# Performance work log

Hardware: AMD Instinct MI355X
Metric: run time of the kernel (lower is better)

## Reference

```python
import jax, jax.numpy as jnp
import numpy as np
from jax import lax

B = 128
HW = 80
NUM_RES_BLOCKS = 3
PC_DIM = 8          # primary capsule dim
PC_CH = 16          # primary capsule channels
DC_DIM = 16         # digit capsule dim
NUM_CLASSES = 10
NUM_PRIMARY = PC_CH * 9 * 9  # 1296


def setup_inputs() -> dict:
    key = jax.random.key(0)
    ks = jax.random.split(key, 16)
    d = {}
    d['x'] = jax.random.normal(ks[0], (B, 1, HW, HW), dtype=jnp.float32)
    # conv1: Conv2d(1, 32, k=3, s=1, p=1) with bias
    d['conv1_w'] = jax.random.normal(ks[1], (32, 1, 3, 3), dtype=jnp.float32) * 0.1
    d['conv1_b'] = jnp.zeros((32,), dtype=jnp.float32)
    d['bn1_g'] = jnp.ones((32,), dtype=jnp.float32)
    d['bn1_b'] = jnp.zeros((32,), dtype=jnp.float32)
    # residual blocks (stacked over block dim): conv1 is 1x1, conv2 is 3x3 pad 1, both bias-free
    d['rb_c1_w'] = jax.random.normal(ks[2], (NUM_RES_BLOCKS, 32, 32, 1, 1), dtype=jnp.float32) * 0.05
    d['rb_bn1_g'] = jnp.ones((NUM_RES_BLOCKS, 32), dtype=jnp.float32)
    d['rb_bn1_b'] = jnp.zeros((NUM_RES_BLOCKS, 32), dtype=jnp.float32)
    d['rb_c2_w'] = jax.random.normal(ks[3], (NUM_RES_BLOCKS, 32, 32, 3, 3), dtype=jnp.float32) * 0.05
    d['rb_bn2_g'] = jnp.ones((NUM_RES_BLOCKS, 32), dtype=jnp.float32)
    d['rb_bn2_b'] = jnp.zeros((NUM_RES_BLOCKS, 32), dtype=jnp.float32)
    # primary capsules: Conv2d(32, 16*8=128, k=9, s=8) with bias
    d['pcaps_w'] = jax.random.normal(ks[4], (PC_CH * PC_DIM, 32, 9, 9), dtype=jnp.float32) * 0.02
    d['pcaps_b'] = jnp.zeros((PC_CH * PC_DIM,), dtype=jnp.float32)
    # routing weights W: original shape (1, 1296, 10, 16, 8); drop broadcast batch dim
    d['W_caps'] = 0.01 * jax.random.normal(ks[5], (NUM_PRIMARY, NUM_CLASSES, DC_DIM, PC_DIM), dtype=jnp.float32)
    return d


def _conv(x, w, stride=1, pad=0):
    return lax.conv_general_dilated(
        x, w, (stride, stride), [(pad, pad), (pad, pad)],
        dimension_numbers=('NCHW', 'OIHW', 'NCHW'))


def _bn(x, g, b, eps=1e-5):
    # training-mode batch norm (batch statistics, biased variance)
    m = jnp.mean(x, axis=(0, 2, 3), keepdims=True)
    v = jnp.var(x, axis=(0, 2, 3), keepdims=True)
    return (x - m) * lax.rsqrt(v + eps) * g[None, :, None, None] + b[None, :, None, None]


def _squash(s, axis=-1):
    n2 = jnp.sum(s * s, axis=axis, keepdims=True)
    return (n2 / (1.0 + n2)) * (s / jnp.sqrt(n2 + 1e-9))


def reference(x, conv1_w, conv1_b, bn1_g, bn1_b,
              rb_c1_w, rb_bn1_g, rb_bn1_b, rb_c2_w, rb_bn2_g, rb_bn2_b,
              pcaps_w, pcaps_b, W_caps):
    h = _conv(x, conv1_w, stride=1, pad=1) + conv1_b[None, :, None, None]
    h = jax.nn.relu(_bn(h, bn1_g, bn1_b))
    for i in range(NUM_RES_BLOCKS):
        idt = h
        o = jax.nn.relu(_bn(_conv(h, rb_c1_w[i]), rb_bn1_g[i], rb_bn1_b[i]))
        o = _bn(_conv(o, rb_c2_w[i], pad=1), rb_bn2_g[i], rb_bn2_b[i])
        h = jax.nn.relu(o + idt)
    # primary capsules -> [B, 128, 9, 9]
    p = _conv(h, pcaps_w, stride=8) + pcaps_b[None, :, None, None]
    bsz = p.shape[0]
    p = p.reshape(bsz, PC_CH, PC_DIM, 9, 9)
    p = jnp.transpose(p, (0, 1, 3, 4, 2)).reshape(bsz, NUM_PRIMARY, PC_DIM)  # [B, 1296, 8]
    # u_hat[b,p,c,d] = W[p,c,d,k] * u[b,p,k]
    u_hat = jnp.einsum('pcdk,bpk->bpcd', W_caps, p)  # [B, 1296, 10, 16]
    # dynamic routing, 3 iterations
    b_log = jnp.zeros((bsz, NUM_PRIMARY, NUM_CLASSES), dtype=u_hat.dtype)
    for r in range(3):
        c = jax.nn.softmax(b_log, axis=2)  # [B, 1296, 10]
        s = jnp.einsum('bpc,bpcd->bcd', c, u_hat)  # [B, 10, 16]
        v = _squash(s, axis=-1)
        if r < 2:
            b_log = b_log + jnp.einsum('bpcd,bcd->bpc', u_hat, v)
    lengths = jnp.sqrt(jnp.sum(v * v, axis=-1) + 1e-9)  # [B, 10]
    return (v, lengths)
```

## Files before the change

kernel.cpp:

```cpp
#include <hip/hip_runtime.h>
#include <hip/hip_bf16.h>
#include <cstddef>


#define B_ 128
#define HW_ 80
#define PIX 6400
#define CHW 204800
#define NPRIM 1296

typedef __attribute__((ext_vector_type(8))) short bf16x8;
typedef __attribute__((ext_vector_type(4))) float f32x4;

__device__ inline float ldH(const unsigned short* p, size_t i) {
  union { unsigned int u; float f; } c; c.u = ((unsigned int)p[i]) << 16; return c.f;
}
__device__ inline float bf16tof(unsigned short u) {
  union { unsigned int uu; float f; } c; c.uu = ((unsigned int)u) << 16; return c.f;
}
__device__ inline float lo16f(unsigned int w) {
  union { unsigned int uu; float f; } c; c.uu = w << 16; return c.f;
}
__device__ inline float hi16f(unsigned int w) {
  union { unsigned int uu; float f; } c; c.uu = w & 0xffff0000u; return c.f;
}
__device__ inline unsigned short ftobf16(float v) {
  __hip_bfloat16 b = __float2bfloat16(v);
  return *reinterpret_cast<unsigned short*>(&b);
}
__device__ inline float stRound(float* p, size_t i, float v) { p[i] = v; return v; }
__device__ inline float stRound(unsigned short* p, size_t i, float v) {
  unsigned short u = ftobf16(v); p[i] = u; return bf16tof(u);
}

__global__ __launch_bounds__(256) void conv1_k(const float* __restrict__ x,
                                               const float* __restrict__ w,
                                               const float* __restrict__ bias,
                                               unsigned short* __restrict__ out,
                                               float* __restrict__ partc) {
  __shared__ float sAB[4 * 64];
  int idx = blockIdx.x * 256 + threadIdx.x;
  int b = idx / PIX, p = idx - b * PIX;
  int y = p / HW_, xx = p - y * HW_;
  const float* xb = x + (size_t)b * PIX;
  float in[3][3];
#pragma unroll
  for (int dy = 0; dy < 3; dy++) {
    int yy = y + dy - 1;
#pragma unroll
    for (int dx = 0; dx < 3; dx++) {
      int xc = xx + dx - 1;
      in[dy][dx] = (yy >= 0 && yy < HW_ && xc >= 0 && xc < HW_) ? xb[yy * HW_ + xc] : 0.f;
    }
  }
  int lane = threadIdx.x & 63, wv = threadIdx.x >> 6;
  size_t obase = (size_t)b * CHW + p;
#pragma unroll 1
  for (int co = 0; co < 32; co++) {
    float a = bias[co];
#pragma unroll
    for (int t = 0; t < 9; t++) a = fmaf(in[t / 3][t % 3], w[co * 9 + t], a);
    float ar = stRound(out, obase + (size_t)co * PIX, a);
    float r = ar, r2 = ar * ar;
#pragma unroll
    for (int off = 32; off > 0; off >>= 1) { r += __shfl_down(r, off); r2 += __shfl_down(r2, off); }
    if (lane == 0) { sAB[wv * 64 + co] = r; sAB[wv * 64 + 32 + co] = r2; }
  }
  __syncthreads();
  if (threadIdx.x < 64) {
    float s = sAB[threadIdx.x] + sAB[64 + threadIdx.x] + sAB[128 + threadIdx.x] + sAB[192 + threadIdx.x];
    partc[(size_t)blockIdx.x * 64 + threadIdx.x] = s;
  }
}

__global__ __launch_bounds__(256) void finC_k(const float* __restrict__ partc,
                                              const float* __restrict__ g,
                                              const float* __restrict__ bb,
                                              float* __restrict__ sb) {
  __shared__ float red[256];
  int co = blockIdx.x;
  int tid = threadIdx.x;
  int half = tid >> 7, t = tid & 127;
  const float* p = partc + (half ? (32 + co) : co);
  float s = 0.f;
  for (int j = t; j < 3200; j += 128) s += p[(size_t)j * 64];
  red[tid] = s;
  __syncthreads();
  for (int st = 64; st > 0; st >>= 1) {
    if (t < st) red[half * 128 + t] += red[half * 128 + t + st];
    __syncthreads();
  }
  if (tid == 0) {
    float sum = red[0], sum2 = red[128];
    const float inv = 1.f / 819200.f;
    float mean = sum * inv;
    float var = sum2 * inv - mean * mean;
    float sc = g[co] * rsqrtf(var + 1e-5f);
    sb[co] = sc;
    sb[32 + co] = bb[co] - mean * sc;
  }
}

template <bool RES, bool STATS1>
__global__ __launch_bounds__(256) void fuse_k(const unsigned short* __restrict__ X,
                                              const unsigned short* __restrict__ Hold,
                                              unsigned short* __restrict__ Hout,
                                              unsigned int* __restrict__ Xa4,
                                              const float* __restrict__ sb,
                                              const float* __restrict__ w1,
                                              float* __restrict__ partc) {
  __shared__ float sAB[4 * 64];
  int idx = blockIdx.x * 256 + threadIdx.x;
  int b = idx / PIX, p = idx - b * PIX;
  size_t base = (size_t)b * CHW + p;
  float h[32];
#pragma unroll
  for (int ci = 0; ci < 32; ci++) {
    float v = bf16tof(X[base + (size_t)ci * PIX]);
    v = fmaf(v, sb[ci], sb[32 + ci]);
    if (RES) v += ldH(Hold, base + (size_t)ci * PIX);
    v = fmaxf(v, 0.f);
    h[ci] = stRound(Hout, base + (size_t)ci * PIX, v);
  }
  if (STATS1) {
    int lane = threadIdx.x & 63, wv = threadIdx.x >> 6;
    unsigned int pk[16];
#pragma unroll
    for (int co = 0; co < 32; co++) {
      float a = 0.f;
#pragma unroll
      for (int ci = 0; ci < 32; ci++) a = fmaf(h[ci], w1[co * 32 + ci], a);
      unsigned short ua = ftobf16(a);
      if (co & 1) pk[co >> 1] |= ((unsigned int)ua) << 16;
      else        pk[co >> 1] = (unsigned int)ua;
      float ar = bf16tof(ua);
      float r = ar, r2 = ar * ar;
#pragma unroll
      for (int off = 32; off > 0; off >>= 1) { r += __shfl_down(r, off); r2 += __shfl_down(r2, off); }
      if (lane == 0) { sAB[wv * 64 + co] = r; sAB[wv * 64 + 32 + co] = r2; }
    }
    uint4* dst = (uint4*)(Xa4 + ((size_t)b * PIX + p) * 16);
#pragma unroll
    for (int q = 0; q < 4; q++) {
      uint4 v;
      v.x = pk[q * 4 + 0]; v.y = pk[q * 4 + 1]; v.z = pk[q * 4 + 2]; v.w = pk[q * 4 + 3];
      dst[q] = v;
    }
    __syncthreads();
    if (threadIdx.x < 64) {
      float s = sAB[threadIdx.x] + sAB[64 + threadIdx.x] + sAB[128 + threadIdx.x] + sAB[192 + threadIdx.x];
      partc[(size_t)blockIdx.x * 64 + threadIdx.x] = s;
    }
  }
}

__global__ __launch_bounds__(256) void wprep_k(const float* __restrict__ pw,
                                               const float* __restrict__ rb3,
                                               unsigned short* __restrict__ wpc,
                                               float* __restrict__ wp) {
  int idx = blockIdx.x * 256 + threadIdx.x;
  if (idx < 331776) {
    int j = idx & 7, co = (idx >> 3) & 127, lg = (idx >> 10) & 3, s = idx >> 12;
    int ci = lg * 8 + j;
    float w = pw[(size_t)co * 2592 + ci * 81 + s];
    unsigned short hi = ftobf16(w);
    wpc[idx] = hi;
    wpc[331776 + idx] = ftobf16(w - bf16tof(hi));
  } else if (idx < 359424) {
    int e2 = idx - 331776;
    int rb = e2 / 9216, e = e2 - rb * 9216;
    unsigned short* wA3 = (unsigned short*)(wp + rb * 9216);
    int j = e & 7, co = (e >> 3) & 31, g = (e >> 8) & 3, t = e >> 10;
    int ci = g * 8 + j;
    float w = rb3[rb * 9216 + (co * 32 + ci) * 9 + t];
    unsigned short hi = ftobf16(w);
    wA3[e] = hi;
    wA3[9216 + e] = ftobf16(w - bf16tof(hi));
  }
}

__global__ __launch_bounds__(256) void conv3_k(const unsigned int* __restrict__ Xa4,
                                               const float* __restrict__ sba,
                                               const unsigned short* __restrict__ wA3,
                                               unsigned short* __restrict__ X,
                                               float* __restrict__ partc) {
  __shared__ unsigned int o1s[16 * 330];
  __shared__ float sAB[4 * 64];
  int tile_id = blockIdx.x;
  int ty0 = (tile_id / 5) * 16, tx0 = (tile_id % 5) * 16;
  int b = blockIdx.y;
  size_t ibase = (size_t)b * CHW;

  for (int px = threadIdx.x; px < 324; px += 256) {
    int iy = px / 18, ix = px - iy * 18;
    int gy = ty0 - 1 + iy, gx = tx0 - 1 + ix;
    bool inimg = (gy >= 0 && gy < HW_ && gx >= 0 && gx < HW_);
    if (inimg) {
      const uint4* src = (const uint4*)(Xa4 + ((size_t)b * PIX + gy * HW_ + gx) * 16);
      uint4 q0 = src[0], q1 = src[1], q2 = src[2], q3 = src[3];
      unsigned int raw[16] = {q0.x, q0.y, q0.z, q0.w, q1.x, q1.y, q1.z, q1.w,
                              q2.x, q2.y, q2.z, q2.w, q3.x, q3.y, q3.z, q3.w};
#pragma unroll
      for (int pr = 0; pr < 16; pr++) {
        float a0 = lo16f(raw[pr]);
        float a1 = hi16f(raw[pr]);
        float o0 = fmaxf(fmaf(a0, sba[2 * pr], sba[32 + 2 * pr]), 0.f);
        float o1v = fmaxf(fmaf(a1, sba[2 * pr + 1], sba[32 + 2 * pr + 1]), 0.f);
        o1s[pr * 330 + px] = (unsigned int)ftobf16(o0) | ((unsigned int)ftobf16(o1v) << 16);
      }
    } else {
#pragma unroll
      for (int pr = 0; pr < 16; pr++) o1s[pr * 330 + px] = 0u;
    }
  }
  __syncthreads();

  int lane = threadIdx.x & 63;
  int wid = threadIdx.x >> 6;
  int l15 = lane & 15, lg = lane >> 4;

  f32x4 acc8[8];
#pragma unroll
  for (int u = 0; u < 8; u++) acc8[u] = f32x4{0.f, 0.f, 0.f, 0.f};

#pragma unroll 1
  for (int t = 0; t < 9; t++) {
    int dy = t / 3, dx = t - dy * 3;
    int abase = ((t * 4 + lg) * 32 + l15) * 8;
    bf16x8 ah0 = *reinterpret_cast<const bf16x8*>(wA3 + abase);
    bf16x8 ah1 = *reinterpret_cast<const bf16x8*>(wA3 + abase + 128);
    bf16x8 al0 = *reinterpret_cast<const bf16x8*>(wA3 + 9216 + abase);
    bf16x8 al1 = *reinterpret_cast<const bf16x8*>(wA3 + 9216 + abase + 128);
#pragma unroll
    for (int s = 0; s < 4; s++) {
      int hpx = (wid * 4 + s + dy) * 18 + l15 + dx;
      int wbase = lg * 4 * 330 + hpx;
      union { unsigned int u[4]; bf16x8 v; } bb;
      bb.u[0] = o1s[wbase];
      bb.u[1] = o1s[wbase + 330];
      bb.u[2] = o1s[wbase + 660];
      bb.u[3] = o1s[wbase + 990];
      acc8[s * 2 + 0] = __builtin_amdgcn_mfma_f32_16x16x32_bf16(ah0, bb.v, acc8[s * 2 + 0], 0, 0, 0);
      acc8[s * 2 + 0] = __builtin_amdgcn_mfma_f32_16x16x32_bf16(al0, bb.v, acc8[s * 2 + 0], 0, 0, 0);
      acc8[s * 2 + 1] = __builtin_amdgcn_mfma_f32_16x16x32_bf16(ah1, bb.v, acc8[s * 2 + 1], 0, 0, 0);
      acc8[s * 2 + 1] = __builtin_amdgcn_mfma_f32_16x16x32_bf16(al1, bb.v, acc8[s * 2 + 1], 0, 0, 0);
    }
  }

  float sacc[2][4], s2acc[2][4];
#pragma unroll
  for (int Mt = 0; Mt < 2; Mt++)
#pragma unroll
    for (int r = 0; r < 4; r++) { sacc[Mt][r] = 0.f; s2acc[Mt][r] = 0.f; }

  int gx = tx0 + l15;
#pragma unroll
  for (int s = 0; s < 4; s++) {
    int gy = ty0 + wid * 4 + s;
#pragma unroll
    for (int Mt = 0; Mt < 2; Mt++) {
#pragma unroll
      for (int r = 0; r < 4; r++) {
        unsigned short uv = ftobf16(acc8[s * 2 + Mt][r]);
        int co = Mt * 16 + lg * 4 + r;
        X[ibase + (size_t)co * PIX + gy * HW_ + gx] = uv;
        float vr = bf16tof(uv);
        sacc[Mt][r] += vr; s2acc[Mt][r] += vr * vr;
      }
    }
  }
#pragma unroll
  for (int off = 1; off < 16; off <<= 1) {
#pragma unroll
    for (int Mt = 0; Mt < 2; Mt++)
#pragma unroll
      for (int r = 0; r < 4; r++) {
        sacc[Mt][r] += __shfl_xor(sacc[Mt][r], off);
        s2acc[Mt][r] += __shfl_xor(s2acc[Mt][r], off);
      }
  }
  if (l15 == 0) {
#pragma unroll
    for (int Mt = 0; Mt < 2; Mt++)
#pragma unroll
      for (int r = 0; r < 4; r++) {
        int co = Mt * 16 + lg * 4 + r;
        sAB[wid * 64 + co] = sacc[Mt][r];
        sAB[wid * 64 + 32 + co] = s2acc[Mt][r];
      }
  }
  __syncthreads();
  if (threadIdx.x < 64) {
    float s = sAB[threadIdx.x] + sAB[64 + threadIdx.x] + sAB[128 + threadIdx.x] + sAB[192 + threadIdx.x];
    partc[((size_t)(b * 25 + tile_id)) * 64 + threadIdx.x] = s;
  }
}

__global__ __launch_bounds__(256) void pcapsm_k(const unsigned short* __restrict__ Hb,
                                                const unsigned short* __restrict__ wpc,
                                                const float* __restrict__ bias,
                                                float* __restrict__ P) {
  __shared__ unsigned int hs[16 * 721];
  int oy = blockIdx.x, b = blockIdx.y;
  for (int i = threadIdx.x; i < 11520; i += 256) {
    int pr = i / 720, rem = i - pr * 720;
    int ky = rem / 80, col = rem - ky * 80;
    size_t src = ((size_t)(b * 32 + 2 * pr) * HW_ + oy * 8 + ky) * HW_ + col;
    unsigned int pk = (unsigned int)Hb[src] | ((unsigned int)Hb[src + PIX] << 16);
    int phys = (col & 7) * 10 + (col >> 3);
    hs[pr * 721 + ky * 80 + phys] = pk;
  }
  __syncthreads();

  int lane = threadIdx.x & 63, wid = threadIdx.x >> 6;
  int l15 = lane & 15, lg = lane >> 4;
  int colb = (l15 < 9) ? l15 * 8 : (l15 - 9) * 8 + 4;

  f32x4 acc[2];
  acc[0] = f32x4{0.f, 0.f, 0.f, 0.f};
  acc[1] = f32x4{0.f, 0.f, 0.f, 0.f};

#pragma unroll 3
  for (int s = 0; s < 81; s++) {
    int ky = s / 9, kx = s - ky * 9;
    int c = colb + kx;
    int phys = (c & 7) * 10 + (c >> 3);
    int wb = ky * 80 + phys;
    union { unsigned int u[4]; bf16x8 v; } bb;
    bb.u[0] = hs[(lg * 4 + 0) * 721 + wb];
    bb.u[1] = hs[(lg * 4 + 1) * 721 + wb];
    bb.u[2] = hs[(lg * 4 + 2) * 721 + wb];
    bb.u[3] = hs[(lg * 4 + 3) * 721 + wb];
#pragma unroll
    for (int m = 0; m < 2; m++) {
      int mt = wid * 2 + m;
      size_t ab = ((size_t)(s * 4 + lg) * 128 + mt * 16 + l15) * 8;
      bf16x8 ahi = *reinterpret_cast<const bf16x8*>(wpc + ab);
      bf16x8 alo = *reinterpret_cast<const bf16x8*>(wpc + 331776 + ab);
      acc[m] = __builtin_amdgcn_mfma_f32_16x16x32_bf16(ahi, bb.v, acc[m], 0, 0, 0);
      acc[m] = __builtin_amdgcn_mfma_f32_16x16x32_bf16(alo, bb.v, acc[m], 0, 0, 0);
    }
  }

  int ox = l15;
  if (ox < 9) {
#pragma unroll
    for (int m = 0; m < 2; m++) {
      int mt = wid * 2 + m;
#pragma unroll
      for (int r = 0; r < 4; r++) {
        int co = mt * 16 + lg * 4 + r;
        int pp = (co >> 3) * 81 + oy * 9 + ox;
        P[((size_t)b * NPRIM + pp) * 8 + (co & 7)] = acc[m][r] + bias[co];
      }
    }
  }
}

__global__ __launch_bounds__(256) void uhat_k(const float* __restrict__ Pp,
                                              const float* __restrict__ W,
                                              unsigned short* __restrict__ UH) {
  int p = blockIdx.x;
  __shared__ __align__(16) float ush[1024];
  for (int i = threadIdx.x; i < 1024; i += 256) {
    int b = i >> 3, k = i & 7;
    ush[i] = Pp[((size_t)b * NPRIM + p) * 8 + k];
  }
  int cdq = threadIdx.x & 31, bg = threadIdx.x >> 5;
  float4 w0[5], w1[5];
#pragma unroll
  for (int j = 0; j < 5; j++) {
    const float4* wp = (const float4*)(W + ((size_t)p * 160 + j * 32 + cdq) * 8);
    w0[j] = wp[0]; w1[j] = wp[1];
  }
  __syncthreads();
#pragma unroll 1
  for (int pass = 0; pass < 16; pass++) {
    int b = pass * 8 + bg;
    const float4* up = (const float4*)(ush + b * 8);
    float4 u0 = up[0], u1 = up[1];
#pragma unroll
    for (int j = 0; j < 5; j++) {
      float a = w0[j].x * u0.x + w0[j].y * u0.y + w0[j].z * u0.z + w0[j].w * u0.w +
                w1[j].x * u1.x + w1[j].y * u1.y + w1[j].z * u1.z + w1[j].w * u1.w;
      UH[((size_t)b * NPRIM + p) * 160 + j * 32 + cdq] = ftobf16(a);
    }
  }
}

__global__ __launch_bounds__(256) void sred0_k(const unsigned short* __restrict__ UH,
                                               float* __restrict__ V) {
  int c = blockIdx.x, b = blockIdx.y;
  int d = threadIdx.x & 15, pg = threadIdx.x >> 4;
  float acc = 0.f;
  for (int p = pg; p < NPRIM; p += 16)
    acc += 0.1f * bf16tof(UH[((size_t)b * NPRIM + p) * 160 + c * 16 + d]);
  __shared__ float red[256];
  red[threadIdx.x] = acc;
  __syncthreads();
  for (int st = 128; st >= 16; st >>= 1) {
    if (threadIdx.x < st) red[threadIdx.x] += red[threadIdx.x + st];
    __syncthreads();
  }
  if (threadIdx.x < 16) {
    float sv = red[threadIdx.x];
    float n2 = sv * sv;
#pragma unroll
    for (int off = 1; off < 16; off <<= 1) n2 += __shfl_xor(n2, off);
    float sc = (n2 / (1.f + n2)) / sqrtf(n2 + 1e-9f);
    V[((size_t)b * 10 + c) * 16 + threadIdx.x] = sv * sc;
  }
}

template <bool FIRST>
__global__ __launch_bounds__(256) void route_k(const unsigned short* __restrict__ UH,
                                               const float* __restrict__ V,
                                               const float* __restrict__ blogin,
                                               float* __restrict__ blogout,
                                               float* __restrict__ SPART) {
  __shared__ float cl[10 * 216];
  __shared__ float vsh[160];
  int seg = blockIdx.x, b = blockIdx.y;
  for (int i = threadIdx.x; i < 160; i += 256) vsh[i] = V[(size_t)b * 160 + i];
  __syncthreads();
  int pl = threadIdx.x;
  if (pl < 216) {
    int p = seg * 216 + pl;
    const uint4* uh4 = (const uint4*)(UH + ((size_t)b * NPRIM + p) * 160);
    float t[10];
#pragma unroll
    for (int c = 0; c < 10; c++) t[c] = 0.f;
#pragma unroll
    for (int j = 0; j < 20; j++) {
      uint4 u = uh4[j];
      int c = j >> 1, d0 = (j & 1) * 8;
      const float* vs = vsh + c * 16 + d0;
      t[c] += lo16f(u.x) * vs[0] + hi16f(u.x) * vs[1] +
              lo16f(u.y) * vs[2] + hi16f(u.y) * vs[3] +
              lo16f(u.z) * vs[4] + hi16f(u.z) * vs[5] +
              lo16f(u.w) * vs[6] + hi16f(u.w) * vs[7];
    }
    if (!FIRST) {
      const float* bi = blogin + ((size_t)b * NPRIM + p) * 10;
#pragma unroll
      for (int c = 0; c < 10; c++) t[c] += bi[c];
    }
    float* bo = blogout + ((size_t)b * NPRIM + p) * 10;
#pragma unroll
    for (int c = 0; c < 10; c++) bo[c] = t[c];
    float mx = -3.4e38f;
#pragma unroll
    for (int c = 0; c < 10; c++) mx = fmaxf(mx, t[c]);
    float sum = 0.f;
    float e[10];
#pragma unroll
    for (int c = 0; c < 10; c++) { e[c] = __expf(t[c] - mx); sum += e[c]; }
    float inv = 1.f / sum;
#pragma unroll
    for (int c = 0; c < 10; c++) cl[c * 216 + pl] = e[c] * inv;
  }
  __syncthreads();
  if (threadIdx.x < 160) {
    int c = threadIdx.x >> 4, d = threadIdx.x & 15;
    const unsigned short* uhc = UH + ((size_t)b * NPRIM + seg * 216) * 160 + c * 16 + d;
    float s = 0.f;
#pragma unroll 4
    for (int q = 0; q < 216; q++) s += cl[c * 216 + q] * bf16tof(uhc[(size_t)q * 160]);
    SPART[((size_t)b * 6 + seg) * 160 + threadIdx.x] = s;
  }
}

template <bool FINAL>
__global__ __launch_bounds__(256) void squashred_k(const float* __restrict__ SPART,
                                                   float* __restrict__ V,
                                                   float* __restrict__ out) {
  int b = blockIdx.x;
  int t = threadIdx.x;
  if (t < 160) {
    float s = 0.f;
#pragma unroll
    for (int seg = 0; seg < 6; seg++) s += SPART[((size_t)b * 6 + seg) * 160 + t];
    float n2 = s * s;
#pragma unroll
    for (int off = 1; off < 16; off <<= 1) n2 += __shfl_xor(n2, off);
    float sc = (n2 / (1.f + n2)) / sqrtf(n2 + 1e-9f);
    float v = s * sc;
    if (FINAL) {
      out[(size_t)b * 160 + t] = v;
      if ((t & 15) == 0) out[20480 + b * 10 + (t >> 4)] = sqrtf(n2 * sc * sc + 1e-9f);
    } else {
      V[(size_t)b * 160 + t] = v;
    }
  }
}

extern "C" void kernel_launch(void* const* d_in, const int* in_sizes, int n_in,
                              void* d_out, int out_size, void* d_ws, size_t ws_size,
                              hipStream_t stream) {
  (void)in_sizes; (void)n_in; (void)out_size; (void)ws_size;
  const float* x        = (const float*)d_in[0];
  const float* conv1_w  = (const float*)d_in[1];
  const float* conv1_b  = (const float*)d_in[2];
  const float* bn1_g    = (const float*)d_in[3];
  const float* bn1_b    = (const float*)d_in[4];
  const float* rb_c1_w  = (const float*)d_in[5];
  const float* rb_bn1_g = (const float*)d_in[6];
  const float* rb_bn1_b = (const float*)d_in[7];
  const float* rb_c2_w  = (const float*)d_in[8];
  const float* rb_bn2_g = (const float*)d_in[9];
  const float* rb_bn2_b = (const float*)d_in[10];
  const float* pcaps_w  = (const float*)d_in[11];
  const float* pcaps_b  = (const float*)d_in[12];
  const float* W_caps   = (const float*)d_in[13];
  float* ws  = (float*)d_ws;
  float* out = (float*)d_out;

  unsigned short* Xb = (unsigned short*)ws;
  unsigned short* Hb = (unsigned short*)(ws + 13107200);
  unsigned int* Xa4  = (unsigned int*)(ws + 26214400);
  unsigned short* WPC = (unsigned short*)(ws + 52428800);
  float* PART = ws + 52428800 + 331776;
  float* SB   = PART + 32768;
  float* P    = SB + 512;
  float* BLOG = P + 1327104;
  float* WP    = P;
  float* PARTC = BLOG;
  unsigned short* UH = (unsigned short*)(ws + 2654208);
  float* SPART = P;
  float* V     = BLOG + 1658880 + 20480;

  wprep_k<<<1404, 256, 0, stream>>>(pcaps_w, rb_c2_w, WPC, WP);
  conv1_k<<<3200, 256, 0, stream>>>(x, conv1_w, conv1_b, Xb, PARTC);
  finC_k<<<32, 256, 0, stream>>>(PARTC, bn1_g, bn1_b, SB + 0);
  fuse_k<false, true><<<3200, 256, 0, stream>>>(Xb, nullptr, Hb, Xa4, SB + 0,
                                                rb_c1_w + 0, PARTC);
  finC_k<<<32, 256, 0, stream>>>(PARTC, rb_bn1_g + 0, rb_bn1_b + 0, SB + 1 * 64);

  for (int i = 0; i < 3; i++) {
    int sa = 1 + 2 * i, sx = 2 + 2 * i;
    conv3_k<<<dim3(25, 128), 256, 0, stream>>>(Xa4, SB + sa * 64,
                                               (unsigned short*)(WP + i * 9216),
                                               Xb, PARTC);
    finC_k<<<32, 256, 0, stream>>>(PARTC, rb_bn2_g + i * 32, rb_bn2_b + i * 32, SB + sx * 64);
    if (i < 2) {
      fuse_k<true, true><<<3200, 256, 0, stream>>>(Xb, Hb, Hb, Xa4, SB + sx * 64,
                                                   rb_c1_w + (i + 1) * 1024, PARTC);
      finC_k<<<32, 256, 0, stream>>>(PARTC, rb_bn1_g + (i + 1) * 32, rb_bn1_b + (i + 1) * 32,
                                     SB + (sx + 1) * 64);
    } else {
      fuse_k<true, false><<<3200, 256, 0, stream>>>(Xb, Hb, Hb, nullptr, SB + sx * 64,
                                                    nullptr, nullptr);
    }
  }

  pcapsm_k<<<dim3(9, 128), 256, 0, stream>>>(Hb, WPC, pcaps_b, P);
  uhat_k<<<1296, 256, 0, stream>>>(P, W_caps, UH);

  sred0_k<<<dim3(10, 128), 256, 0, stream>>>(UH, V);
  route_k<true><<<dim3(6, 128), 256, 0, stream>>>(UH, V, nullptr, BLOG, SPART);
  squashred_k<false><<<128, 256, 0, stream>>>(SPART, V, nullptr);
  route_k<false><<<dim3(6, 128), 256, 0, stream>>>(UH, V, BLOG, BLOG, SPART);
  squashred_k<true><<<128, 256, 0, stream>>>(SPART, nullptr, out);
}
```

Baseline: 711.7 us.

## Compute residual 1x1 conv with bf16 split-precision MFMA in fuse kernel

Replaces the per-thread scalar 32x32 FMA loop for the 1x1 conv in fuse_k with MFMA 16x16x32 bf16 instructions. Activations are staged through shared memory, and weights are pre-split into hi/lo bf16 pairs by wprep_k to keep near-fp32 accuracy. BN statistics are now reduced with xor shuffles over 16 lanes instead of a full-wave reduction per output channel. The intent is to remove the heavy scalar FMA and shuffle work, at the cost of extra LDS traffic, a second barrier, and a changed workspace layout for the weights.

Result: faster. 587.7 us (-17.4%).

```diff
diff --git a/kernel.cpp b/kernel.cpp
--- a/kernel.cpp
+++ b/kernel.cpp
@@ -107,10 +107,10 @@
                                               unsigned short* __restrict__ Hout,
                                               unsigned int* __restrict__ Xa4,
                                               const float* __restrict__ sb,
-                                              const float* __restrict__ w1,
+                                              const unsigned short* __restrict__ wf1,
                                               float* __restrict__ partc) {
-  __shared__ float sAB[4 * 64];
-  int idx = blockIdx.x * 256 + threadIdx.x;
+  int tid = threadIdx.x;
+  int idx = blockIdx.x * 256 + tid;
   int b = idx / PIX, p = idx - b * PIX;
   size_t base = (size_t)b * CHW + p;
   float h[32];
@@ -123,39 +123,106 @@
     h[ci] = stRound(Hout, base + (size_t)ci * PIX, v);
   }
   if (STATS1) {
-    int lane = threadIdx.x & 63, wv = threadIdx.x >> 6;
-    unsigned int pk[16];
-#pragma unroll
-    for (int co = 0; co < 32; co++) {
-      float a = 0.f;
-#pragma unroll
-      for (int ci = 0; ci < 32; ci++) a = fmaf(h[ci], w1[co * 32 + ci], a);
-      unsigned short ua = ftobf16(a);
-      if (co & 1) pk[co >> 1] |= ((unsigned int)ua) << 16;
-      else        pk[co >> 1] = (unsigned int)ua;
-      float ar = bf16tof(ua);
-      float r = ar, r2 = ar * ar;
-#pragma unroll
-      for (int off = 32; off > 0; off >>= 1) { r += __shfl_down(r, off); r2 += __shfl_down(r2, off); }
-      if (lane == 0) { sAB[wv * 64 + co] = r; sAB[wv * 64 + 32 + co] = r2; }
-    }
-    uint4* dst = (uint4*)(Xa4 + ((size_t)b * PIX + p) * 16);
-#pragma unroll
-    for (int q = 0; q < 4; q++) {
-      uint4 v;
-      v.x = pk[q * 4 + 0]; v.y = pk[q * 4 + 1]; v.z = pk[q * 4 + 2]; v.w = pk[q * 4 + 3];
-      dst[q] = v;
+    __shared__ unsigned int hls[16 * 260];
+    __shared__ float sAB[4 * 64];
+#pragma unroll
+    for (int pr = 0; pr < 16; pr++) {
+      unsigned int pk = (unsigned int)ftobf16(h[2 * pr]) |
+                        ((unsigned int)ftobf16(h[2 * pr + 1]) << 16);
+      hls[pr * 260 + tid] = pk;
     }
     __syncthreads();
-    if (threadIdx.x < 64) {
-      float s = sAB[threadIdx.x] + sAB[64 + threadIdx.x] + sAB[128 + threadIdx.x] + sAB[192 + threadIdx.x];
-      partc[(size_t)blockIdx.x * 64 + threadIdx.x] = s;
+
+    int lane = tid & 63, wv = tid >> 6;
+    int l15 = lane & 15, lg = (lane >> 4) & 3;
+    int pbase = p - tid;
+
+    bf16x8 ah[2], al[2];
+#pragma unroll
+    for (int mt = 0; mt < 2; mt++) {
+      size_t ab = ((size_t)(mt * 4 + lg) * 16 + l15) * 8;
+      ah[mt] = *reinterpret_cast<const bf16x8*>(wf1 + ab);
+      al[mt] = *reinterpret_cast<const bf16x8*>(wf1 + 1024 + ab);
+    }
+
+    f32x4 acc[4][2];
+#pragma unroll
+    for (int nt = 0; nt < 4; nt++)
+#pragma unroll
+      for (int mt = 0; mt < 2; mt++) acc[nt][mt] = f32x4{0.f, 0.f, 0.f, 0.f};
+
+#pragma unroll
+    for (int nt = 0; nt < 4; nt++) {
+      int px = wv * 64 + nt * 16 + l15;
+      union { unsigned int u[4]; bf16x8 v; } bb;
+      bb.u[0] = hls[(lg * 4 + 0) * 260 + px];
+      bb.u[1] = hls[(lg * 4 + 1) * 260 + px];
+      bb.u[2] = hls[(lg * 4 + 2) * 260 + px];
+      bb.u[3] = hls[(lg * 4 + 3) * 260 + px];
+#pragma unroll
+      for (int mt = 0; mt < 2; mt++) {
+        acc[nt][mt] = __builtin_amdgcn_mfma_f32_16x16x32_bf16(ah[mt], bb.v, acc[nt][mt], 0, 0, 0);
+        acc[nt][mt] = __builtin_amdgcn_mfma_f32_16x16x32_bf16(al[mt], bb.v, acc[nt][mt], 0, 0, 0);
+      }
+    }
+
+    float sacc[2][4], s2acc[2][4];
+#pragma unroll
+    for (int mt = 0; mt < 2; mt++)
+#pragma unroll
+      for (int r = 0; r < 4; r++) { sacc[mt][r] = 0.f; s2acc[mt][r] = 0.f; }
+
+#pragma unroll
+    for (int nt = 0; nt < 4; nt++) {
+      int px = wv * 64 + nt * 16 + l15;
+      size_t xb4 = ((size_t)b * PIX + pbase + px) * 16;
+#pragma unroll
+      for (int mt = 0; mt < 2; mt++) {
+        unsigned short u0 = ftobf16(acc[nt][mt][0]);
+        unsigned short u1 = ftobf16(acc[nt][mt][1]);
+        unsigned short u2 = ftobf16(acc[nt][mt][2]);
+        unsigned short u3 = ftobf16(acc[nt][mt][3]);
+        int pi = mt * 8 + lg * 2;
+        Xa4[xb4 + pi] = (unsigned int)u0 | ((unsigned int)u1 << 16);
+        Xa4[xb4 + pi + 1] = (unsigned int)u2 | ((unsigned int)u3 << 16);
+        float v0 = bf16tof(u0), v1 = bf16tof(u1), v2 = bf16tof(u2), v3 = bf16tof(u3);
+        sacc[mt][0] += v0; s2acc[mt][0] += v0 * v0;
+        sacc[mt][1] += v1; s2acc[mt][1] += v1 * v1;
+        sacc[mt][2] += v2; s2acc[mt][2] += v2 * v2;
+        sacc[mt][3] += v3; s2acc[mt][3] += v3 * v3;
+      }
+    }
+#pragma unroll
+    for (int off = 1; off < 16; off <<= 1) {
+#pragma unroll
+      for (int mt = 0; mt < 2; mt++)
+#pragma unroll
+        for (int r = 0; r < 4; r++) {
+          sacc[mt][r] += __shfl_xor(sacc[mt][r], off);
+          s2acc[mt][r] += __shfl_xor(s2acc[mt][r], off);
+        }
+    }
+    if (l15 == 0) {
+#pragma unroll
+      for (int mt = 0; mt < 2; mt++)
+#pragma unroll
+        for (int r = 0; r < 4; r++) {
+          int co = mt * 16 + lg * 4 + r;
+          sAB[wv * 64 + co] = sacc[mt][r];
+          sAB[wv * 64 + 32 + co] = s2acc[mt][r];
+        }
+    }
+    __syncthreads();
+    if (tid < 64) {
+      float s = sAB[tid] + sAB[64 + tid] + sAB[128 + tid] + sAB[192 + tid];
+      partc[(size_t)blockIdx.x * 64 + tid] = s;
     }
   }
 }
 
 __global__ __launch_bounds__(256) void wprep_k(const float* __restrict__ pw,
                                                const float* __restrict__ rb3,
+                                               const float* __restrict__ rb1,
                                                unsigned short* __restrict__ wpc,
                                                float* __restrict__ wp) {
   int idx = blockIdx.x * 256 + threadIdx.x;
@@ -169,13 +236,23 @@
   } else if (idx < 359424) {
     int e2 = idx - 331776;
     int rb = e2 / 9216, e = e2 - rb * 9216;
-    unsigned short* wA3 = (unsigned short*)(wp + rb * 9216);
+    unsigned short* wA3 = (unsigned short*)(wp + rb * 10240);
     int j = e & 7, co = (e >> 3) & 31, g = (e >> 8) & 3, t = e >> 10;
     int ci = g * 8 + j;
     float w = rb3[rb * 9216 + (co * 32 + ci) * 9 + t];
     unsigned short hi = ftobf16(w);
     wA3[e] = hi;
     wA3[9216 + e] = ftobf16(w - bf16tof(hi));
+  } else if (idx < 362496) {
+    int e3 = idx - 359424;
+    int rb = e3 / 1024, t = e3 - rb * 1024;
+    unsigned short* wf1 = (unsigned short*)(wp + rb * 10240 + 9216);
+    int j = t & 7, l15 = (t >> 3) & 15, lg = (t >> 7) & 3, mt = t >> 9;
+    int co = mt * 16 + l15, ci = lg * 8 + j;
+    float w = rb1[rb * 1024 + co * 32 + ci];
+    unsigned short hi = ftobf16(w);
+    wf1[t] = hi;
+    wf1[1024 + t] = ftobf16(w - bf16tof(hi));
   }
 }
 
@@ -529,22 +606,23 @@
   float* SPART = P;
   float* V     = BLOG + 1658880 + 20480;
 
-  wprep_k<<<1404, 256, 0, stream>>>(pcaps_w, rb_c2_w, WPC, WP);
+  wprep_k<<<1416, 256, 0, stream>>>(pcaps_w, rb_c2_w, rb_c1_w, WPC, WP);
   conv1_k<<<3200, 256, 0, stream>>>(x, conv1_w, conv1_b, Xb, PARTC);
   finC_k<<<32, 256, 0, stream>>>(PARTC, bn1_g, bn1_b, SB + 0);
   fuse_k<false, true><<<3200, 256, 0, stream>>>(Xb, nullptr, Hb, Xa4, SB + 0,
-                                                rb_c1_w + 0, PARTC);
+                                                (unsigned short*)(WP + 0 * 10240 + 9216), PARTC);
   finC_k<<<32, 256, 0, stream>>>(PARTC, rb_bn1_g + 0, rb_bn1_b + 0, SB + 1 * 64);
 
   for (int i = 0; i < 3; i++) {
     int sa = 1 + 2 * i, sx = 2 + 2 * i;
     conv3_k<<<dim3(25, 128), 256, 0, stream>>>(Xa4, SB + sa * 64,
-                                               (unsigned short*)(WP + i * 9216),
+                                               (unsigned short*)(WP + i * 10240),
                                                Xb, PARTC);
     finC_k<<<32, 256, 0, stream>>>(PARTC, rb_bn2_g + i * 32, rb_bn2_b + i * 32, SB + sx * 64);
     if (i < 2) {
       fuse_k<true, true><<<3200, 256, 0, stream>>>(Xb, Hb, Hb, Xa4, SB + sx * 64,
-                                                   rb_c1_w + (i + 1) * 1024, PARTC);
+                                                   (unsigned short*)(WP + (i + 1) * 10240 + 9216),
+                                                   PARTC);
       finC_k<<<32, 256, 0, stream>>>(PARTC, rb_bn1_g + (i + 1) * 32, rb_bn1_b + (i + 1) * 32,
                                      SB + (sx + 1) * 64);
     } else {
```
